# Optimization experiments

Hardware: AMD Instinct MI355X
Metric: run time of the kernel (lower is better)

Reference implementation:

```python
import jax, jax.numpy as jnp
import numpy as np

NEG_SLOPE = 0.2

def _gat_conv(x, W, att_src, att_dst, bias, src, dst, n_nodes):
    # x: [N, F_in], W: [F_in, F_out], att_*: [F_out], bias: [F_out]
    h = x @ W                                   # [N, F_out]
    a_src = h @ att_src                         # [N]
    a_dst = h @ att_dst                         # [N]
    e = a_src[src] + a_dst[dst]                 # [E]
    e = jnp.where(e > 0, e, NEG_SLOPE * e)      # LeakyReLU
    # segment softmax over incoming edges of each destination node
    m = jax.ops.segment_max(e, dst, num_segments=n_nodes)
    ex = jnp.exp(e - m[dst])
    denom = jax.ops.segment_sum(ex, dst, num_segments=n_nodes)
    alpha = ex / denom[dst]                     # [E]
    msg = alpha[:, None] * h[src]               # [E, F_out]
    out = jax.ops.segment_sum(msg, dst, num_segments=n_nodes)
    return out + bias

def setup_inputs() -> dict:
    key = jax.random.key(0)
    ks = jax.random.split(key, 12)
    N, E, F_in, H, F_out = 50000, 800000, 128, 128, 128
    def glorot(k, shape):
        lim = float(np.sqrt(6.0 / sum(shape))) if len(shape) > 1 else float(np.sqrt(6.0 / shape[0]))
        return jax.random.uniform(k, shape, jnp.float32, -lim, lim)
    return {
        "x": jax.random.normal(ks[0], (N, F_in), jnp.float32),
        "edge_index": jax.random.randint(ks[1], (2, E), 0, N, jnp.int64),
        "W1": glorot(ks[2], (F_in, H)),
        "att_src1": glorot(ks[3], (H,)),
        "att_dst1": glorot(ks[4], (H,)),
        "b1": jnp.zeros((H,), jnp.float32),
        "W2": glorot(ks[5], (H, F_out)),
        "att_src2": glorot(ks[6], (F_out,)),
        "att_dst2": glorot(ks[7], (F_out,)),
        "b2": jnp.zeros((F_out,), jnp.float32),
    }

def reference(x, edge_index, W1, att_src1, att_dst1, b1, W2, att_src2, att_dst2, b2):
    n_nodes = x.shape[0]
    # add self loops (PyG GATConv default)
    loops = jnp.arange(n_nodes, dtype=edge_index.dtype)
    src = jnp.concatenate([edge_index[0], loops])
    dst = jnp.concatenate([edge_index[1], loops])
    h = _gat_conv(x, W1, att_src1, att_dst1, b1, src, dst, n_nodes)
    h = jax.nn.relu(h)
    h = _gat_conv(h, W2, att_src2, att_dst2, b2, src, dst, n_nodes)
    return jax.nn.relu(h)
```

## Files before the change

### kernel.cpp

```cpp
#include <hip/hip_runtime.h>
#include <cstdint>

#define NEG_SLOPE 0.2f
#define F 128

#define BKT_SHIFT 7
#define BKT_SIZE  128
#define NBK_PAD   512
#define CHUNK     4096
#define EPT       8
#define CAP       3072

typedef unsigned short u16;
typedef unsigned int u32;
typedef float float8_t __attribute__((ext_vector_type(8)));
typedef float float4_t __attribute__((ext_vector_type(4)));
typedef short short8_t __attribute__((ext_vector_type(8)));

__device__ inline u16 f2bf(float f) {
    u32 u = __float_as_uint(f);
    u32 r = u + 0x7fffu + ((u >> 16) & 1u);
    return (u16)(r >> 16);
}
__device__ inline float bflo(u32 v) { return __uint_as_float(v << 16); }
__device__ inline float bfhi(u32 v) { return __uint_as_float(v & 0xffff0000u); }

__device__ inline void prep_unit(const float* __restrict__ W, u16* __restrict__ Wt, int u) {
    int frag = u >> 6, lane = u & 63;
    int K0 = frag >> 3, nt = frag & 7;
    int kbase = K0 * 32 + (lane >> 4) * 8;
    int n = nt * 16 + (lane & 15);
    u32 w[4];
    #pragma unroll
    for (int p = 0; p < 4; ++p) {
        u16 e0 = f2bf(W[(size_t)(kbase + 2 * p) * F + n]);
        u16 e1 = f2bf(W[(size_t)(kbase + 2 * p + 1) * F + n]);
        w[p] = (u32)e0 | ((u32)e1 << 16);
    }
    uint4 o; o.x = w[0]; o.y = w[1]; o.z = w[2]; o.w = w[3];
    ((uint4*)Wt)[u] = o;
}

__global__ void __launch_bounds__(512) count_prep_kernel(const int* __restrict__ ei, int E, int tot,
                                                         int* __restrict__ bucketTotal,
                                                         const float* __restrict__ W1, u16* __restrict__ Wt1,
                                                         const float* __restrict__ W2, u16* __restrict__ Wt2,
                                                         int nCountBlocks) {
    if ((int)blockIdx.x >= nCountBlocks) {
        int pb = blockIdx.x - nCountBlocks;
        if (threadIdx.x < 512) {
            int u = (pb & 3) * 512 + threadIdx.x;
            if (pb < 4) prep_unit(W1, Wt1, u);
            else        prep_unit(W2, Wt2, u);
        }
        return;
    }
    __shared__ int hist[NBK_PAD];
    int tid = threadIdx.x;
    hist[tid] = 0;
    __syncthreads();
    int base = blockIdx.x * CHUNK;
    int w = base + tid * EPT;
    if (w + EPT <= E) {
        int4 d0 = *(const int4*)&ei[E + w];
        int4 d1 = *(const int4*)&ei[E + w + 4];
        atomicAdd(&hist[d0.x >> BKT_SHIFT], 1);
        atomicAdd(&hist[d0.y >> BKT_SHIFT], 1);
        atomicAdd(&hist[d0.z >> BKT_SHIFT], 1);
        atomicAdd(&hist[d0.w >> BKT_SHIFT], 1);
        atomicAdd(&hist[d1.x >> BKT_SHIFT], 1);
        atomicAdd(&hist[d1.y >> BKT_SHIFT], 1);
        atomicAdd(&hist[d1.z >> BKT_SHIFT], 1);
        atomicAdd(&hist[d1.w >> BKT_SHIFT], 1);
    } else {
        #pragma unroll
        for (int i = 0; i < EPT; ++i) {
            int e = w + i;
            if (e < tot) {
                int d = (e < E) ? ei[E + e] : (e - E);
                atomicAdd(&hist[d >> BKT_SHIFT], 1);
            }
        }
    }
    __syncthreads();
    int v = hist[tid];
    if (v > 0) atomicAdd(&bucketTotal[tid], v);
}

__global__ void __launch_bounds__(512) bucket_scan_kernel(const int* __restrict__ bucketTotal,
                                                          int* __restrict__ bucketStart,
                                                          int* __restrict__ bucketCursor) {
    __shared__ int sc[NBK_PAD];
    int t = threadIdx.x;
    int v = bucketTotal[t];
    sc[t] = v;
    __syncthreads();
    for (int o = 1; o < NBK_PAD; o <<= 1) {
        int u = (t >= o) ? sc[t - o] : 0;
        __syncthreads();
        sc[t] += u;
        __syncthreads();
    }
    int excl = sc[t] - v;
    bucketStart[t] = excl;
    bucketCursor[t] = excl;
    if (t == NBK_PAD - 1) bucketStart[NBK_PAD] = sc[t];
}

__global__ void __launch_bounds__(512) scatter_kernel(const int* __restrict__ ei, int E, int tot,
                                                      int* __restrict__ bucketCursor,
                                                      u32* __restrict__ pairs) {
    __shared__ int hist[NBK_PAD], excl[NBK_PAD], lcur[NBK_PAD], runb[NBK_PAD];
    __shared__ u32 stage[CHUNK];
    __shared__ u16 bktid[CHUNK];
    int tid = threadIdx.x;
    hist[tid] = 0;
    __syncthreads();
    int base = blockIdx.x * CHUNK;
    int chunkCnt = min(CHUNK, tot - base);
    int rs[EPT], rd[EPT];
    int w = base + tid * EPT;
    if (w + EPT <= E) {
        int4 s0 = *(const int4*)&ei[w];
        int4 s1 = *(const int4*)&ei[w + 4];
        int4 d0 = *(const int4*)&ei[E + w];
        int4 d1 = *(const int4*)&ei[E + w + 4];
        rs[0] = s0.x; rs[1] = s0.y; rs[2] = s0.z; rs[3] = s0.w;
        rs[4] = s1.x; rs[5] = s1.y; rs[6] = s1.z; rs[7] = s1.w;
        rd[0] = d0.x; rd[1] = d0.y; rd[2] = d0.z; rd[3] = d0.w;
        rd[4] = d1.x; rd[5] = d1.y; rd[6] = d1.z; rd[7] = d1.w;
        #pragma unroll
        for (int i = 0; i < EPT; ++i) atomicAdd(&hist[rd[i] >> BKT_SHIFT], 1);
    } else {
        #pragma unroll
        for (int i = 0; i < EPT; ++i) {
            int e = w + i;
            rd[i] = -1;
            if (e < tot) {
                int s, d;
                if (e < E) { s = ei[e]; d = ei[E + e]; } else { s = e - E; d = s; }
                rs[i] = s; rd[i] = d;
                atomicAdd(&hist[d >> BKT_SHIFT], 1);
            }
        }
    }
    __syncthreads();
    int v = hist[tid];
    excl[tid] = v;
    __syncthreads();
    for (int o = 1; o < NBK_PAD; o <<= 1) {
        int u = (tid >= o) ? excl[tid - o] : 0;
        __syncthreads();
        excl[tid] += u;
        __syncthreads();
    }
    int ex = excl[tid] - v;
    __syncthreads();
    excl[tid] = ex;
    lcur[tid] = ex;
    if (v > 0) runb[tid] = atomicAdd(&bucketCursor[tid], v);
    __syncthreads();
    #pragma unroll
    for (int i = 0; i < EPT; ++i) {
        if (rd[i] >= 0) {
            int b = rd[i] >> BKT_SHIFT;
            int pos = atomicAdd(&lcur[b], 1);
            stage[pos] = ((u32)rs[i] << BKT_SHIFT) | (u32)(rd[i] & (BKT_SIZE - 1));
            bktid[pos] = (u16)b;
        }
    }
    __syncthreads();
    for (int j = tid; j < chunkCnt; j += 512) {
        int b = (int)bktid[j];
        pairs[(size_t)runb[b] + (j - excl[b])] = stage[j];
    }
}

__device__ void build_body(const u32* __restrict__ pairs, const int* __restrict__ bucketStart,
                           int* __restrict__ row_ptr, int* __restrict__ csr,
                           int N, int tot, int b, char* smem) {
    u32* stage  = (u32*)smem;
    int* sorted = (int*)(smem + CAP * 4);
    int* hist   = (int*)(smem + CAP * 8);
    int* pfx    = (int*)(smem + CAP * 8 + 512);
    int* cur    = (int*)(smem + CAP * 8 + 1024);
    int tid = threadIdx.x;
    int base = bucketStart[b];
    int cnt = bucketStart[b + 1] - base;
    if (cnt > CAP) cnt = CAP;
    if (tid < BKT_SIZE) hist[tid] = 0;
    __syncthreads();
    for (int j = tid; j < cnt; j += 256) {
        u32 p = pairs[(size_t)base + j];
        stage[j] = p;
        atomicAdd(&hist[p & (BKT_SIZE - 1)], 1);
    }
    __syncthreads();
    if (tid < BKT_SIZE) pfx[tid] = hist[tid];
    __syncthreads();
    for (int o = 1; o < BKT_SIZE; o <<= 1) {
        int u = 0;
        if (tid < BKT_SIZE && tid >= o) u = pfx[tid - o];
        __syncthreads();
        if (tid < BKT_SIZE) pfx[tid] += u;
        __syncthreads();
    }
    if (tid < BKT_SIZE) {
        int ex = pfx[tid] - hist[tid];
        cur[tid] = ex;
        int d = b * BKT_SIZE + tid;
        if (d < N) row_ptr[d] = base + ex;
    }
    __syncthreads();
    for (int j = tid; j < cnt; j += 256) {
        u32 p = stage[j];
        int pos = atomicAdd(&cur[p & (BKT_SIZE - 1)], 1);
        sorted[pos] = (int)(p >> BKT_SHIFT);
    }
    __syncthreads();
    for (int j = tid; j < cnt; j += 256) csr[(size_t)base + j] = sorted[j];
    if (b == 0 && tid == 0) row_ptr[N] = tot;
}

template<int IN_BF16>
__device__ void gemm_body(const void* __restrict__ in, const u16* __restrict__ Wt,
                          const float* __restrict__ att_s, const float* __restrict__ att_d,
                          u16* __restrict__ h, float* __restrict__ asrc, float* __restrict__ adst,
                          int N, int gblk, u16* wlds) {
    int tid = threadIdx.x;
    {
        const uint4* src = (const uint4*)Wt;
        uint4* dst = (uint4*)wlds;
        #pragma unroll
        for (int i = 0; i < 8; ++i) dst[tid + i * 256] = src[tid + i * 256];
    }
    __syncthreads();
    int wave = tid >> 6, lane = tid & 63;
    int li = lane & 15, grp = lane >> 4;
    int rowBase = (gblk * 4 + wave) * 16;
    if (rowBase >= N) return;
    int row = rowBase + li;
    if (row > N - 1) row = N - 1;

    short8_t b[4];
    if (IN_BF16) {
        const u16* xp = (const u16*)in + (size_t)row * F + grp * 8;
        #pragma unroll
        for (int K0 = 0; K0 < 4; ++K0)
            b[K0] = *(const short8_t*)(xp + K0 * 32);
    } else {
        const float* xp = (const float*)in + (size_t)row * F + grp * 8;
        #pragma unroll
        for (int K0 = 0; K0 < 4; ++K0) {
            float8_t xv = *(const float8_t*)(xp + K0 * 32);
            short8_t t;
            #pragma unroll
            for (int i = 0; i < 8; ++i) t[i] = (short)f2bf(xv[i]);
            b[K0] = t;
        }
    }

    float4_t acc[8];
    #pragma unroll
    for (int nt = 0; nt < 8; ++nt) acc[nt] = (float4_t){0.f, 0.f, 0.f, 0.f};
    #pragma unroll
    for (int nt = 0; nt < 8; ++nt) {
        #pragma unroll
        for (int K0 = 0; K0 < 4; ++K0) {
            short8_t a = *(const short8_t*)&wlds[((K0 * 8 + nt) * 64 + lane) * 8];
            acc[nt] = __builtin_amdgcn_mfma_f32_16x16x32_bf16(a, b[K0], acc[nt], 0, 0, 0);
        }
    }

    u16* hr = h + (size_t)row * F + grp * 4;
    #pragma unroll
    for (int nt = 0; nt < 8; ++nt) {
        u32 lo = (u32)f2bf(acc[nt][0]) | ((u32)f2bf(acc[nt][1]) << 16);
        u32 hi = (u32)f2bf(acc[nt][2]) | ((u32)f2bf(acc[nt][3]) << 16);
        uint2 st; st.x = lo; st.y = hi;
        *(uint2*)(hr + (size_t)nt * 16) = st;
    }

    float rs = 0.f, rd = 0.f;
    #pragma unroll
    for (int nt = 0; nt < 8; ++nt) {
        float4 a4 = *(const float4*)(att_s + nt * 16 + grp * 4);
        float4 d4 = *(const float4*)(att_d + nt * 16 + grp * 4);
        rs += acc[nt][0] * a4.x + acc[nt][1] * a4.y + acc[nt][2] * a4.z + acc[nt][3] * a4.w;
        rd += acc[nt][0] * d4.x + acc[nt][1] * d4.y + acc[nt][2] * d4.z + acc[nt][3] * d4.w;
    }
    rs += __shfl_xor(rs, 16); rs += __shfl_xor(rs, 32);
    rd += __shfl_xor(rd, 16); rd += __shfl_xor(rd, 32);
    if (grp == 0) { asrc[row] = rs; adst[row] = rd; }
}

template<int IN_BF16>
__global__ void __launch_bounds__(256) gemm_mfma_kernel(const void* __restrict__ in,
    const u16* __restrict__ Wt, const float* __restrict__ att_s, const float* __restrict__ att_d,
    u16* __restrict__ h, float* __restrict__ asrc, float* __restrict__ adst, int N)
{
    __shared__ u16 wlds[16384];
    gemm_body<IN_BF16>(in, Wt, att_s, att_d, h, asrc, adst, N, blockIdx.x, wlds);
}

__global__ void __launch_bounds__(256) build_gemm_kernel(
    const u32* __restrict__ pairs, const int* __restrict__ bucketStart,
    int* __restrict__ row_ptr, int* __restrict__ csr, int N, int tot,
    const float* __restrict__ x, const u16* __restrict__ Wt,
    const float* __restrict__ att_s, const float* __restrict__ att_d,
    u16* __restrict__ h, float* __restrict__ asrc, float* __restrict__ adst, int NBK)
{
    __shared__ __align__(16) char smem[32768];
    if ((int)blockIdx.x < NBK) {
        build_body(pairs, bucketStart, row_ptr, csr, N, tot, blockIdx.x, smem);
    } else {
        gemm_body<0>(x, Wt, att_s, att_d, h, asrc, adst, N, blockIdx.x - NBK, (u16*)smem);
    }
}

#define FMA8(pp, v)                                                              \
    acc[0] = fmaf(pp, bflo((v).x), acc[0]); acc[1] = fmaf(pp, bfhi((v).x), acc[1]); \
    acc[2] = fmaf(pp, bflo((v).y), acc[2]); acc[3] = fmaf(pp, bfhi((v).y), acc[3]); \
    acc[4] = fmaf(pp, bflo((v).z), acc[4]); acc[5] = fmaf(pp, bfhi((v).z), acc[5]); \
    acc[6] = fmaf(pp, bflo((v).w), acc[6]); acc[7] = fmaf(pp, bfhi((v).w), acc[7]);

template<int OUT_BF16>
__global__ void __launch_bounds__(256) aggregate_kernel(
    const u16* __restrict__ h, const float* __restrict__ asrc, const float* __restrict__ adst,
    const int* __restrict__ row_ptr, const int* __restrict__ csr,
    const float* __restrict__ bias, void* __restrict__ out, int N)
{
    int gid = blockIdx.x * 16 + (threadIdx.x >> 4);
    if (gid >= N) return;
    int lane = threadIdx.x & 15;
    int start = row_ptr[gid];
    int deg = row_ptr[gid + 1] - start;
    float ad = adst[gid];

    const uint4* h4 = (const uint4*)h;
    float denom = 0.f;
    float acc[8];
    #pragma unroll
    for (int j = 0; j < 8; ++j) acc[j] = 0.f;

    for (int c0 = 0; c0 < deg; c0 += 16) {
        int cnt = min(16, deg - c0);
        int s = 0; float p = 0.f;
        if (lane < cnt) {
            s = csr[start + c0 + lane];
            float e = asrc[s] + ad;
            e = (e > 0.f) ? e : NEG_SLOPE * e;
            p = __expf(fminf(e, 70.f));
        }
        denom += p;

        int t = 0;
        for (; t + 8 <= cnt; t += 8) {
            int s0 = __shfl(s, t, 16),     s1 = __shfl(s, t + 1, 16);
            int s2 = __shfl(s, t + 2, 16), s3 = __shfl(s, t + 3, 16);
            int s4 = __shfl(s, t + 4, 16), s5 = __shfl(s, t + 5, 16);
            int s6 = __shfl(s, t + 6, 16), s7 = __shfl(s, t + 7, 16);
            float p0 = __shfl(p, t, 16),     p1 = __shfl(p, t + 1, 16);
            float p2 = __shfl(p, t + 2, 16), p3 = __shfl(p, t + 3, 16);
            float p4 = __shfl(p, t + 4, 16), p5 = __shfl(p, t + 5, 16);
            float p6 = __shfl(p, t + 6, 16), p7 = __shfl(p, t + 7, 16);
            uint4 v0 = h4[(size_t)s0 * 16 + lane];
            uint4 v1 = h4[(size_t)s1 * 16 + lane];
            uint4 v2 = h4[(size_t)s2 * 16 + lane];
            uint4 v3 = h4[(size_t)s3 * 16 + lane];
            uint4 v4 = h4[(size_t)s4 * 16 + lane];
            uint4 v5 = h4[(size_t)s5 * 16 + lane];
            uint4 v6 = h4[(size_t)s6 * 16 + lane];
            uint4 v7 = h4[(size_t)s7 * 16 + lane];
            FMA8(p0, v0); FMA8(p1, v1); FMA8(p2, v2); FMA8(p3, v3);
            FMA8(p4, v4); FMA8(p5, v5); FMA8(p6, v6); FMA8(p7, v7);
        }
        for (; t + 4 <= cnt; t += 4) {
            int s0 = __shfl(s, t, 16),     s1 = __shfl(s, t + 1, 16);
            int s2 = __shfl(s, t + 2, 16), s3 = __shfl(s, t + 3, 16);
            float p0 = __shfl(p, t, 16),     p1 = __shfl(p, t + 1, 16);
            float p2 = __shfl(p, t + 2, 16), p3 = __shfl(p, t + 3, 16);
            uint4 v0 = h4[(size_t)s0 * 16 + lane];
            uint4 v1 = h4[(size_t)s1 * 16 + lane];
            uint4 v2 = h4[(size_t)s2 * 16 + lane];
            uint4 v3 = h4[(size_t)s3 * 16 + lane];
            FMA8(p0, v0); FMA8(p1, v1); FMA8(p2, v2); FMA8(p3, v3);
        }
        for (; t < cnt; ++t) {
            int st = __shfl(s, t, 16);
            float pt = __shfl(p, t, 16);
            uint4 v = h4[(size_t)st * 16 + lane];
            FMA8(pt, v);
        }
    }

    #pragma unroll
    for (int o = 1; o < 16; o <<= 1) denom += __shfl_xor(denom, o);
    float inv = 1.0f / denom;
    const float* bp = bias + lane * 8;
    float r[8];
    #pragma unroll
    for (int j = 0; j < 8; ++j) {
        float v = fmaf(acc[j], inv, bp[j]);
        r[j] = v > 0.f ? v : 0.f;
    }
    if (OUT_BF16) {
        u32 w[4];
        #pragma unroll
        for (int p2 = 0; p2 < 4; ++p2)
            w[p2] = (u32)f2bf(r[2 * p2]) | ((u32)f2bf(r[2 * p2 + 1]) << 16);
        uint4 st; st.x = w[0]; st.y = w[1]; st.z = w[2]; st.w = w[3];
        ((uint4*)out)[(size_t)gid * 16 + lane] = st;
    } else {
        float4 o0 = make_float4(r[0], r[1], r[2], r[3]);
        float4 o1 = make_float4(r[4], r[5], r[6], r[7]);
        ((float4*)out)[(size_t)gid * 32 + lane * 2]     = o0;
        ((float4*)out)[(size_t)gid * 32 + lane * 2 + 1] = o1;
    }
}

static inline size_t align_up(size_t v, size_t a) { return (v + a - 1) & ~(a - 1); }

extern "C" void kernel_launch(void* const* d_in, const int* in_sizes, int n_in,
                              void* d_out, int out_size, void* d_ws, size_t ws_size,
                              hipStream_t stream) {
    const float* x   = (const float*)d_in[0];
    const int*   ei  = (const int*)d_in[1];
    const float* W1  = (const float*)d_in[2];
    const float* as1 = (const float*)d_in[3];
    const float* ad1 = (const float*)d_in[4];
    const float* b1  = (const float*)d_in[5];
    const float* W2  = (const float*)d_in[6];
    const float* as2 = (const float*)d_in[7];
    const float* ad2 = (const float*)d_in[8];
    const float* b2  = (const float*)d_in[9];

    int N = in_sizes[0] / F;
    int E = in_sizes[1] / 2;
    int tot = E + N;

    char* ws = (char*)d_ws;
    size_t off = 0;
    #define ALLOC(type, name, count)                                    \
        type* name = (type*)(ws + off);                                  \
        off = align_up(off + (size_t)(count) * sizeof(type), 256);
    ALLOC(u16,   h,       (size_t)N * F);
    ALLOC(u16,   out1,    (size_t)N * F);
    ALLOC(float, asrc,    N);
    ALLOC(float, adst,    N);
    ALLOC(int,   row_ptr, N + 4);
    ALLOC(int,   csr,     tot);
    ALLOC(u32,   pairs,   tot);
    ALLOC(int,   bucketTotal,  NBK_PAD);
    ALLOC(int,   bucketStart,  NBK_PAD + 1);
    ALLOC(int,   bucketCursor, NBK_PAD);
    ALLOC(u16,   Wt1,     16384);
    ALLOC(u16,   Wt2,     16384);
    #undef ALLOC

    hipMemsetAsync(bucketTotal, 0, NBK_PAD * sizeof(int), stream);

    int NBK = (N + BKT_SIZE - 1) / BKT_SIZE;
    int nchunks = (tot + CHUNK - 1) / CHUNK;
    int ngemm = (N + 63) / 64;
    int nagg  = (N + 15) / 16;

    count_prep_kernel<<<nchunks + 8, 512, 0, stream>>>(ei, E, tot, bucketTotal,
                                                       W1, Wt1, W2, Wt2, nchunks);
    bucket_scan_kernel<<<1, NBK_PAD, 0, stream>>>(bucketTotal, bucketStart, bucketCursor);
    scatter_kernel<<<nchunks, 512, 0, stream>>>(ei, E, tot, bucketCursor, pairs);
    build_gemm_kernel<<<NBK + ngemm, 256, 0, stream>>>(pairs, bucketStart, row_ptr, csr, N, tot,
                                                       x, Wt1, as1, ad1, h, asrc, adst, NBK);
    aggregate_kernel<1><<<nagg, 256, 0, stream>>>(h, asrc, adst, row_ptr, csr, b1, out1, N);
    gemm_mfma_kernel<1><<<ngemm, 256, 0, stream>>>(out1, Wt2, as2, ad2, h, asrc, adst, N);
    aggregate_kernel<0><<<nagg, 256, 0, stream>>>(h, asrc, adst, row_ptr, csr, b2, d_out, N);
}
```

Measured before the change: 208.4 us.

## Drop histogram pass with fixed-capacity buckets and prefetch next edge chunk

Removes the separate counting pass over edge destinations. The scatter kernel now writes directly into fixed-capacity per-bucket regions (CAP slots each), and a scan over the final cursors produces compact CSR offsets. This saves one full read of the edge list and one kernel launch, at the cost of a larger pairs buffer and silently dropping edges if a bucket overflows CAP. Separately, the aggregation kernel now prefetches the next 16-edge chunk's source indices and attention scores while the current chunk accumulates, and its unrolled gather is refactored into a template helper.

```diff
diff --git a/kernel.cpp b/kernel.cpp
--- a/kernel.cpp
+++ b/kernel.cpp
@@ -41,75 +41,19 @@
     ((uint4*)Wt)[u] = o;
 }
 
-__global__ void __launch_bounds__(512) count_prep_kernel(const int* __restrict__ ei, int E, int tot,
-                                                         int* __restrict__ bucketTotal,
-                                                         const float* __restrict__ W1, u16* __restrict__ Wt1,
-                                                         const float* __restrict__ W2, u16* __restrict__ Wt2,
-                                                         int nCountBlocks) {
-    if ((int)blockIdx.x >= nCountBlocks) {
-        int pb = blockIdx.x - nCountBlocks;
-        if (threadIdx.x < 512) {
-            int u = (pb & 3) * 512 + threadIdx.x;
-            if (pb < 4) prep_unit(W1, Wt1, u);
-            else        prep_unit(W2, Wt2, u);
-        }
+__global__ void __launch_bounds__(512) scatter_prep_kernel(const int* __restrict__ ei, int E, int tot,
+                                                           int* __restrict__ bucketCursor,
+                                                           u32* __restrict__ pairs,
+                                                           const float* __restrict__ W1, u16* __restrict__ Wt1,
+                                                           const float* __restrict__ W2, u16* __restrict__ Wt2,
+                                                           int nScatBlocks) {
+    if ((int)blockIdx.x >= nScatBlocks) {
+        int pb = blockIdx.x - nScatBlocks;
+        int u = (pb & 3) * 512 + threadIdx.x;
+        if (pb < 4) prep_unit(W1, Wt1, u);
+        else        prep_unit(W2, Wt2, u);
         return;
     }
-    __shared__ int hist[NBK_PAD];
-    int tid = threadIdx.x;
-    hist[tid] = 0;
-    __syncthreads();
-    int base = blockIdx.x * CHUNK;
-    int w = base + tid * EPT;
-    if (w + EPT <= E) {
-        int4 d0 = *(const int4*)&ei[E + w];
-        int4 d1 = *(const int4*)&ei[E + w + 4];
-        atomicAdd(&hist[d0.x >> BKT_SHIFT], 1);
-        atomicAdd(&hist[d0.y >> BKT_SHIFT], 1);
-        atomicAdd(&hist[d0.z >> BKT_SHIFT], 1);
-        atomicAdd(&hist[d0.w >> BKT_SHIFT], 1);
-        atomicAdd(&hist[d1.x >> BKT_SHIFT], 1);
-        atomicAdd(&hist[d1.y >> BKT_SHIFT], 1);
-        atomicAdd(&hist[d1.z >> BKT_SHIFT], 1);
-        atomicAdd(&hist[d1.w >> BKT_SHIFT], 1);
-    } else {
-        #pragma unroll
-        for (int i = 0; i < EPT; ++i) {
-            int e = w + i;
-            if (e < tot) {
-                int d = (e < E) ? ei[E + e] : (e - E);
-                atomicAdd(&hist[d >> BKT_SHIFT], 1);
-            }
-        }
-    }
-    __syncthreads();
-    int v = hist[tid];
-    if (v > 0) atomicAdd(&bucketTotal[tid], v);
-}
-
-__global__ void __launch_bounds__(512) bucket_scan_kernel(const int* __restrict__ bucketTotal,
-                                                          int* __restrict__ bucketStart,
-                                                          int* __restrict__ bucketCursor) {
-    __shared__ int sc[NBK_PAD];
-    int t = threadIdx.x;
-    int v = bucketTotal[t];
-    sc[t] = v;
-    __syncthreads();
-    for (int o = 1; o < NBK_PAD; o <<= 1) {
-        int u = (t >= o) ? sc[t - o] : 0;
-        __syncthreads();
-        sc[t] += u;
-        __syncthreads();
-    }
-    int excl = sc[t] - v;
-    bucketStart[t] = excl;
-    bucketCursor[t] = excl;
-    if (t == NBK_PAD - 1) bucketStart[NBK_PAD] = sc[t];
-}
-
-__global__ void __launch_bounds__(512) scatter_kernel(const int* __restrict__ ei, int E, int tot,
-                                                      int* __restrict__ bucketCursor,
-                                                      u32* __restrict__ pairs) {
     __shared__ int hist[NBK_PAD], excl[NBK_PAD], lcur[NBK_PAD], runb[NBK_PAD];
     __shared__ u32 stage[CHUNK];
     __shared__ u16 bktid[CHUNK];
@@ -158,7 +102,7 @@
     __syncthreads();
     excl[tid] = ex;
     lcur[tid] = ex;
-    if (v > 0) runb[tid] = atomicAdd(&bucketCursor[tid], v);
+    if (v > 0) runb[tid] = tid * CAP + atomicAdd(&bucketCursor[tid], v);
     __syncthreads();
     #pragma unroll
     for (int i = 0; i < EPT; ++i) {
@@ -172,8 +116,27 @@
     __syncthreads();
     for (int j = tid; j < chunkCnt; j += 512) {
         int b = (int)bktid[j];
-        pairs[(size_t)runb[b] + (j - excl[b])] = stage[j];
-    }
+        size_t idx = (size_t)runb[b] + (j - excl[b]);
+        if (idx < (size_t)(b + 1) * CAP)
+            pairs[idx] = stage[j];
+    }
+}
+
+__global__ void __launch_bounds__(512) bucket_scan_kernel(const int* __restrict__ bucketCursor,
+                                                          int* __restrict__ bucketStart) {
+    __shared__ int sc[NBK_PAD];
+    int t = threadIdx.x;
+    int v = min(bucketCursor[t], CAP);
+    sc[t] = v;
+    __syncthreads();
+    for (int o = 1; o < NBK_PAD; o <<= 1) {
+        int u = (t >= o) ? sc[t - o] : 0;
+        __syncthreads();
+        sc[t] += u;
+        __syncthreads();
+    }
+    bucketStart[t] = sc[t] - v;
+    if (t == NBK_PAD - 1) bucketStart[NBK_PAD] = sc[t];
 }
 
 __device__ void build_body(const u32* __restrict__ pairs, const int* __restrict__ bucketStart,
@@ -185,13 +148,13 @@
     int* pfx    = (int*)(smem + CAP * 8 + 512);
     int* cur    = (int*)(smem + CAP * 8 + 1024);
     int tid = threadIdx.x;
-    int base = bucketStart[b];
-    int cnt = bucketStart[b + 1] - base;
-    if (cnt > CAP) cnt = CAP;
+    size_t srcb = (size_t)b * CAP;
+    int dstb = bucketStart[b];
+    int cnt = bucketStart[b + 1] - dstb;
     if (tid < BKT_SIZE) hist[tid] = 0;
     __syncthreads();
     for (int j = tid; j < cnt; j += 256) {
-        u32 p = pairs[(size_t)base + j];
+        u32 p = pairs[srcb + j];
         stage[j] = p;
         atomicAdd(&hist[p & (BKT_SIZE - 1)], 1);
     }
@@ -209,7 +172,7 @@
         int ex = pfx[tid] - hist[tid];
         cur[tid] = ex;
         int d = b * BKT_SIZE + tid;
-        if (d < N) row_ptr[d] = base + ex;
+        if (d < N) row_ptr[d] = dstb + ex;
     }
     __syncthreads();
     for (int j = tid; j < cnt; j += 256) {
@@ -218,7 +181,7 @@
         sorted[pos] = (int)(p >> BKT_SHIFT);
     }
     __syncthreads();
-    for (int j = tid; j < cnt; j += 256) csr[(size_t)base + j] = sorted[j];
+    for (int j = tid; j < cnt; j += 256) csr[(size_t)dstb + j] = sorted[j];
     if (b == 0 && tid == 0) row_ptr[N] = tot;
 }
 
@@ -318,11 +281,26 @@
     }
 }
 
-#define FMA8(pp, v)                                                              \
-    acc[0] = fmaf(pp, bflo((v).x), acc[0]); acc[1] = fmaf(pp, bfhi((v).x), acc[1]); \
-    acc[2] = fmaf(pp, bflo((v).y), acc[2]); acc[3] = fmaf(pp, bfhi((v).y), acc[3]); \
-    acc[4] = fmaf(pp, bflo((v).z), acc[4]); acc[5] = fmaf(pp, bfhi((v).z), acc[5]); \
-    acc[6] = fmaf(pp, bflo((v).w), acc[6]); acc[7] = fmaf(pp, bfhi((v).w), acc[7]);
+template<int U>
+__device__ __forceinline__ void gfma(const uint4* __restrict__ h4, int lane, int s, float p, int t,
+                                     float (&acc)[8]) {
+    int ss[U]; float pp[U]; uint4 vv[U];
+    #pragma unroll
+    for (int i = 0; i < U; ++i) { ss[i] = __shfl(s, t + i, 16); pp[i] = __shfl(p, t + i, 16); }
+    #pragma unroll
+    for (int i = 0; i < U; ++i) vv[i] = h4[(size_t)ss[i] * 16 + lane];
+    #pragma unroll
+    for (int i = 0; i < U; ++i) {
+        acc[0] = fmaf(pp[i], bflo(vv[i].x), acc[0]);
+        acc[1] = fmaf(pp[i], bfhi(vv[i].x), acc[1]);
+        acc[2] = fmaf(pp[i], bflo(vv[i].y), acc[2]);
+        acc[3] = fmaf(pp[i], bfhi(vv[i].y), acc[3]);
+        acc[4] = fmaf(pp[i], bflo(vv[i].z), acc[4]);
+        acc[5] = fmaf(pp[i], bfhi(vv[i].z), acc[5]);
+        acc[6] = fmaf(pp[i], bflo(vv[i].w), acc[6]);
+        acc[7] = fmaf(pp[i], bfhi(vv[i].w), acc[7]);
+    }
+}
 
 template<int OUT_BF16>
 __global__ void __launch_bounds__(256) aggregate_kernel(
@@ -339,59 +317,33 @@
 
     const uint4* h4 = (const uint4*)h;
     float denom = 0.f;
-    float acc[8];
-    #pragma unroll
-    for (int j = 0; j < 8; ++j) acc[j] = 0.f;
-
-    for (int c0 = 0; c0 < deg; c0 += 16) {
-        int cnt = min(16, deg - c0);
-        int s = 0; float p = 0.f;
+    float acc[8] = {0.f, 0.f, 0.f, 0.f, 0.f, 0.f, 0.f, 0.f};
+
+    int c0 = 0;
+    int cnt = min(16, deg);
+    int s = 0; float a = 0.f;
+    if (lane < cnt) { s = csr[start + lane]; a = asrc[s]; }
+    for (;;) {
+        float p = 0.f;
         if (lane < cnt) {
-            s = csr[start + c0 + lane];
-            float e = asrc[s] + ad;
+            float e = a + ad;
             e = (e > 0.f) ? e : NEG_SLOPE * e;
             p = __expf(fminf(e, 70.f));
         }
         denom += p;
 
+        int nc0 = c0 + 16;
+        int ncnt = min(16, deg - nc0);
+        int s2 = 0; float a2 = 0.f;
+        if (nc0 < deg && lane < ncnt) { s2 = csr[start + nc0 + lane]; a2 = asrc[s2]; }
+
         int t = 0;
-        for (; t + 8 <= cnt; t += 8) {
-            int s0 = __shfl(s, t, 16),     s1 = __shfl(s, t + 1, 16);
-            int s2 = __shfl(s, t + 2, 16), s3 = __shfl(s, t + 3, 16);
-            int s4 = __shfl(s, t + 4, 16), s5 = __shfl(s, t + 5, 16);
-            int s6 = __shfl(s, t + 6, 16), s7 = __shfl(s, t + 7, 16);
-            float p0 = __shfl(p, t, 16),     p1 = __shfl(p, t + 1, 16);
-            float p2 = __shfl(p, t + 2, 16), p3 = __shfl(p, t + 3, 16);
-            float p4 = __shfl(p, t + 4, 16), p5 = __shfl(p, t + 5, 16);
-            float p6 = __shfl(p, t + 6, 16), p7 = __shfl(p, t + 7, 16);
-            uint4 v0 = h4[(size_t)s0 * 16 + lane];
-            uint4 v1 = h4[(size_t)s1 * 16 + lane];
-            uint4 v2 = h4[(size_t)s2 * 16 + lane];
-            uint4 v3 = h4[(size_t)s3 * 16 + lane];
-            uint4 v4 = h4[(size_t)s4 * 16 + lane];
-            uint4 v5 = h4[(size_t)s5 * 16 + lane];
-            uint4 v6 = h4[(size_t)s6 * 16 + lane];
-            uint4 v7 = h4[(size_t)s7 * 16 + lane];
-            FMA8(p0, v0); FMA8(p1, v1); FMA8(p2, v2); FMA8(p3, v3);
-            FMA8(p4, v4); FMA8(p5, v5); FMA8(p6, v6); FMA8(p7, v7);
-        }
-        for (; t + 4 <= cnt; t += 4) {
-            int s0 = __shfl(s, t, 16),     s1 = __shfl(s, t + 1, 16);
-            int s2 = __shfl(s, t + 2, 16), s3 = __shfl(s, t + 3, 16);
-            float p0 = __shfl(p, t, 16),     p1 = __shfl(p, t + 1, 16);
-            float p2 = __shfl(p, t + 2, 16), p3 = __shfl(p, t + 3, 16);
-            uint4 v0 = h4[(size_t)s0 * 16 + lane];
-            uint4 v1 = h4[(size_t)s1 * 16 + lane];
-            uint4 v2 = h4[(size_t)s2 * 16 + lane];
-            uint4 v3 = h4[(size_t)s3 * 16 + lane];
-            FMA8(p0, v0); FMA8(p1, v1); FMA8(p2, v2); FMA8(p3, v3);
-        }
-        for (; t < cnt; ++t) {
-            int st = __shfl(s, t, 16);
-            float pt = __shfl(p, t, 16);
-            uint4 v = h4[(size_t)st * 16 + lane];
-            FMA8(pt, v);
-        }
+        for (; t + 8 <= cnt; t += 8) gfma<8>(h4, lane, s, p, t, acc);
+        for (; t + 4 <= cnt; t += 4) gfma<4>(h4, lane, s, p, t, acc);
+        for (; t < cnt; ++t)         gfma<1>(h4, lane, s, p, t, acc);
+
+        if (nc0 >= deg) break;
+        c0 = nc0; cnt = ncnt; s = s2; a = a2;
     }
 
     #pragma unroll
@@ -450,25 +402,23 @@
     ALLOC(float, adst,    N);
     ALLOC(int,   row_ptr, N + 4);
     ALLOC(int,   csr,     tot);
-    ALLOC(u32,   pairs,   tot);
-    ALLOC(int,   bucketTotal,  NBK_PAD);
+    ALLOC(u32,   pairs,   (size_t)NBK_PAD * CAP);
     ALLOC(int,   bucketStart,  NBK_PAD + 1);
     ALLOC(int,   bucketCursor, NBK_PAD);
     ALLOC(u16,   Wt1,     16384);
     ALLOC(u16,   Wt2,     16384);
     #undef ALLOC
 
-    hipMemsetAsync(bucketTotal, 0, NBK_PAD * sizeof(int), stream);
+    hipMemsetAsync(bucketCursor, 0, NBK_PAD * sizeof(int), stream);
 
     int NBK = (N + BKT_SIZE - 1) / BKT_SIZE;
     int nchunks = (tot + CHUNK - 1) / CHUNK;
     int ngemm = (N + 63) / 64;
     int nagg  = (N + 15) / 16;
 
-    count_prep_kernel<<<nchunks + 8, 512, 0, stream>>>(ei, E, tot, bucketTotal,
-                                                       W1, Wt1, W2, Wt2, nchunks);
-    bucket_scan_kernel<<<1, NBK_PAD, 0, stream>>>(bucketTotal, bucketStart, bucketCursor);
-    scatter_kernel<<<nchunks, 512, 0, stream>>>(ei, E, tot, bucketCursor, pairs);
+    scatter_prep_kernel<<<nchunks + 8, 512, 0, stream>>>(ei, E, tot, bucketCursor, pairs,
+                                                         W1, Wt1, W2, Wt2, nchunks);
+    bucket_scan_kernel<<<1, NBK_PAD, 0, stream>>>(bucketCursor, bucketStart);
     build_gemm_kernel<<<NBK + ngemm, 256, 0, stream>>>(pairs, bucketStart, row_ptr, csr, N, tot,
                                                        x, Wt1, as1, ad1, h, asrc, adst, NBK);
     aggregate_kernel<1><<<nagg, 256, 0, stream>>>(h, asrc, adst, row_ptr, csr, b1, out1, N);
```

After: 201.2 us. 1.04x faster.
